# Optimization experiments

Hardware: AMD Instinct MI355X
Metric: run time of the kernel (lower is better)

## Reference

```python
import jax, jax.numpy as jnp
import numpy as np

B = 32; NPG = 290; N = B * NPG; EPG = 2320; E = B * EPG
LP = 900; IN_FEATS = 75; D = 128; HD = 256; K = 3; HK = HD * K; HOUT = 2


def setup_inputs() -> dict:
    key = jax.random.key(0)
    ks = jax.random.split(key, 20)
    s = 0.05
    rng = np.random.default_rng(0)
    off = np.arange(B)[:, None] * NPG  # keep edges inside each graph block
    edge_src = jnp.asarray((rng.integers(0, NPG, (B, EPG)) + off).reshape(-1), dtype=jnp.int32)
    edge_dst = jnp.asarray((rng.integers(0, NPG, (B, EPG)) + off).reshape(-1), dtype=jnp.int32)
    node_h = jax.random.normal(ks[0], (N, IN_FEATS), jnp.float32)
    v_p = jax.random.randint(ks[1], (B, LP), 0, 26, jnp.int32)
    W_init = (jax.random.normal(ks[2], (IN_FEATS, D)) * s).at[:, -1].set(0.0)  # padding unit zeroed
    gcn_W = jax.random.normal(ks[3], (3, 3, D, D)) * s
    gcn_b = jnp.zeros((3, 3, D))
    gcn_Wres = jax.random.normal(ks[4], (3, 3, D, D)) * s
    gcn_bres = jnp.zeros((3, 3, D))
    emb = (jax.random.normal(ks[5], (26, D)) * s).at[0].set(0.0)  # padding_idx=0
    conv1_w = jax.random.normal(ks[6], (D, D, 3)) * s
    conv2_w = jax.random.normal(ks[7], (D, D, 6)) * s
    conv3_w = jax.random.normal(ks[8], (D, D, 9)) * s
    conv_b = jnp.zeros((3, D))
    cnn_bn_g = jnp.ones((3, D)); cnn_bn_b = jnp.zeros((3, D))
    Wv = jax.random.normal(ks[9], (D, HK)) * s; bv = jnp.zeros((HK,))
    Wq = jax.random.normal(ks[10], (D, HK)) * s; bq = jnp.zeros((HK,))
    h_mat = jax.random.normal(ks[11], (HOUT, HK)) * s
    h_bias = jnp.zeros((HOUT,))
    ban_bn_g = jnp.ones((HD,)); ban_bn_b = jnp.zeros((HD,))
    m_w1 = jax.random.normal(ks[12], (HD, 512)) * s; m_b1 = jnp.zeros((512,))
    m_w2 = jax.random.normal(ks[13], (512, 512)) * s; m_b2 = jnp.zeros((512,))
    m_w3 = jax.random.normal(ks[14], (512, 128)) * s; m_b3 = jnp.zeros((128,))
    m_w4 = jax.random.normal(ks[15], (128, 1)) * s; m_b4 = jnp.zeros((1,))
    mbn_g1 = jnp.ones((512,)); mbn_b1 = jnp.zeros((512,))
    mbn_g2 = jnp.ones((512,)); mbn_b2 = jnp.zeros((512,))
    mbn_g3 = jnp.ones((128,)); mbn_b3 = jnp.zeros((128,))
    return dict(node_h=node_h, edge_src=edge_src, edge_dst=edge_dst, v_p=v_p,
                W_init=W_init, gcn_W=gcn_W, gcn_b=gcn_b, gcn_Wres=gcn_Wres, gcn_bres=gcn_bres,
                emb=emb, conv1_w=conv1_w, conv2_w=conv2_w, conv3_w=conv3_w, conv_b=conv_b,
                cnn_bn_g=cnn_bn_g, cnn_bn_b=cnn_bn_b, Wv=Wv, bv=bv, Wq=Wq, bq=bq,
                h_mat=h_mat, h_bias=h_bias, ban_bn_g=ban_bn_g, ban_bn_b=ban_bn_b,
                m_w1=m_w1, m_b1=m_b1, m_w2=m_w2, m_b2=m_b2, m_w3=m_w3, m_b3=m_b3,
                m_w4=m_w4, m_b4=m_b4, mbn_g1=mbn_g1, mbn_b1=mbn_b1, mbn_g2=mbn_g2,
                mbn_b2=mbn_b2, mbn_g3=mbn_g3, mbn_b3=mbn_b3)


def _bn_feat(x, g, b):  # BatchNorm1d on [B, C], training-mode batch stats
    m = jnp.mean(x, 0); v = jnp.var(x, 0)
    return (x - m) * jax.lax.rsqrt(v + 1e-5) * g + b


def _bn_chan(x, g, b):  # BatchNorm1d on [B, C, L]
    m = jnp.mean(x, (0, 2), keepdims=True); v = jnp.var(x, (0, 2), keepdims=True)
    return (x - m) * jax.lax.rsqrt(v + 1e-5) * g[None, :, None] + b[None, :, None]


def _forward(node_h, W_init, gcn_W, gcn_b, gcn_Wres, gcn_bres, emb, conv1_w, conv2_w,
             conv3_w, conv_b, cnn_bn_g, cnn_bn_b, Wv, bv, Wq, bq, h_mat, h_bias,
             ban_bn_g, ban_bn_b, m_w1, m_b1, m_w2, m_b2, m_w3, m_b3, m_w4, m_b4,
             mbn_g1, mbn_b1, mbn_g2, mbn_b2, mbn_g3, mbn_b3, edge_src, edge_dst, v_p):
    relu = jax.nn.relu

    def gcn(h, W, b, Wr, br):  # 3 dgllife GCN layers: sum-aggregate + relu + residual
        for l in range(3):
            agg = jax.ops.segment_sum(h[edge_src], edge_dst, num_segments=N)
            h = relu(agg @ W[l] + b[l]) + relu(h @ Wr[l] + br[l])
        return h

    h0 = node_h @ W_init  # shared init_transform (no bias)
    v_d_o = gcn(h0, gcn_W[0], gcn_b[0], gcn_Wres[0], gcn_bres[0]).reshape(B, NPG, D)
    pos1 = gcn(h0, gcn_W[1], gcn_b[1], gcn_Wres[1], gcn_bres[1]).reshape(B, NPG, D)
    pos2 = gcn(h0, gcn_W[2], gcn_b[2], gcn_Wres[2], gcn_bres[2]).reshape(B, NPG, D)

    x = emb[v_p].transpose(0, 2, 1)  # [B, D, LP]
    dn = ('NCH', 'OIH', 'NCH')
    for w, cb, g, bb in ((conv1_w, conv_b[0], cnn_bn_g[0], cnn_bn_b[0]),
                         (conv2_w, conv_b[1], cnn_bn_g[1], cnn_bn_b[1]),
                         (conv3_w, conv_b[2], cnn_bn_g[2], cnn_bn_b[2])):
        x = jax.lax.conv_general_dilated(x, w, (1,), 'VALID', dimension_numbers=dn) + cb[None, :, None]
        x = _bn_chan(relu(x), g, bb)
    v_p_o = x.transpose(0, 2, 1)  # [B, 885, D]

    q_ = relu(v_p_o @ Wq + bq)  # BAN q_net (shared across views)

    def ban(vd):  # BANLayer forward (eval-mode dropout)
        v_ = relu(vd @ Wv + bv)  # [B, Nv, HK]
        att = jnp.einsum('hk,bvk,bqk->bhvq', h_mat, v_, q_) + h_bias[None, :, None, None]
        f = jnp.einsum('bvk,bhvq,bqk->bk', v_, att, q_)  # summed over h_out heads
        f = f.reshape(-1, HD, K).sum(-1)  # AvgPool1d(k) * k == sum over k groups
        return _bn_feat(f, ban_bn_g, ban_bn_b)

    def mlp(f):
        f = _bn_feat(relu(f @ m_w1 + m_b1), mbn_g1, mbn_b1)
        f = _bn_feat(relu(f @ m_w2 + m_b2), mbn_g2, mbn_b2)
        f = _bn_feat(relu(f @ m_w3 + m_b3), mbn_g3, mbn_b3)
        return f @ m_w4 + m_b4

    f_o = ban(v_d_o)  # Transformer_lar treated as identity -> beta blend is a no-op
    score_o = mlp(f_o)
    s1 = mlp(ban(pos1))
    s2 = mlp(ban(pos2))

    def norm(z):
        return z / jnp.maximum(jnp.linalg.norm(z, axis=1, keepdims=True), 1e-12)

    km = norm(s1) @ norm(s2).T  # cosine_similarity_kernel
    loss = -jnp.mean(jnp.diagonal(jax.nn.log_softmax(km, axis=1)))  # CE vs arange labels
    return jnp.concatenate([score_o, s1, s2, loss * jnp.ones((B, 1), score_o.dtype)], axis=1)


def reference(node_h, edge_src, edge_dst, v_p, W_init, gcn_W, gcn_b, gcn_Wres, gcn_bres,
              emb, conv1_w, conv2_w, conv3_w, conv_b, cnn_bn_g, cnn_bn_b, Wv, bv, Wq, bq,
              h_mat, h_bias, ban_bn_g, ban_bn_b, m_w1, m_b1, m_w2, m_b2, m_w3, m_b3,
              m_w4, m_b4, mbn_g1, mbn_b1, mbn_g2, mbn_b2, mbn_g3, mbn_b3):
    return _forward(node_h, W_init, gcn_W, gcn_b, gcn_Wres, gcn_bres, emb, conv1_w,
                    conv2_w, conv3_w, conv_b, cnn_bn_g, cnn_bn_b, Wv, bv, Wq, bq,
                    h_mat, h_bias, ban_bn_g, ban_bn_b, m_w1, m_b1, m_w2, m_b2, m_w3,
                    m_b3, m_w4, m_b4, mbn_g1, mbn_b1, mbn_g2, mbn_b2, mbn_g3, mbn_b3,
                    edge_src, edge_dst, v_p)
```

## Files before the change

### kernel.cpp

```cpp
#include <hip/hip_runtime.h>
#include <hip/hip_bf16.h>

#define Bc 32
#define NPGc 290
#define Nn 9280
#define Ec 74240
#define LPc 900
#define INFc 75
#define Dd 128
#define HKc 768
#define LQ 885
#define LQP 896
#define S1 904
#define S2 896
#define S3 888
#define NT 78
#define TSZ 4096

typedef __attribute__((ext_vector_type(8))) short bf16x8;
typedef __attribute__((ext_vector_type(16))) float f32x16;

static __device__ __forceinline__ unsigned short f2bf(float v){
  unsigned int u = __float_as_uint(v);
  unsigned int r = u + 0x7FFFu + ((u >> 16) & 1u);
  return (unsigned short)(r >> 16);
}
static __device__ __forceinline__ float bf2f(unsigned short b){
  return __uint_as_float(((unsigned int)b) << 16);
}

__global__ void k_sentinel(float* out, float val){
  int t = threadIdx.x;
  if (t < 128) out[t] = val;
}

__global__ void k_h0(float* __restrict__ h0, const float* __restrict__ nh, const float* __restrict__ Wi){
  int n = blockIdx.x, j = threadIdx.x;
  __shared__ float arow[INFc];
  if (j < INFc) arow[j] = nh[(size_t)n*INFc + j];
  __syncthreads();
  float s = 0.f;
  #pragma unroll 5
  for (int k=0;k<INFc;k++) s += arow[k]*Wi[(size_t)k*Dd + j];
  h0[(size_t)n*Dd + j] = s;
}

__global__ void k_build_adj(float* __restrict__ A, const int* __restrict__ src, const int* __restrict__ dst){
  int e = blockIdx.x*blockDim.x + threadIdx.x;
  if (e >= Ec) return;
  int s = src[e], d = dst[e];
  int b = d / NPGc;
  int dl = d - b*NPGc, sl = s - b*NPGc;
  atomicAdd(&A[((size_t)b*NPGc + dl)*NPGc + sl], 1.f);
}

__global__ void k_wsplit(unsigned short* __restrict__ dstW, unsigned short* __restrict__ dstWr,
                         const float* __restrict__ W, const float* __restrict__ Wr){
  int idx = blockIdx.x*256 + threadIdx.x;
  if (idx >= 9*Dd*Dd) return;
  int gl = idx >> 14;
  int r  = idx & 16383;
  int k  = r >> 7, j = r & 127;
  int c = k >> 4, slot = k & 15;
  size_t o = ((((size_t)gl*8 + c)*Dd + j) << 4) + slot;
  const size_t NW = (size_t)9*8*Dd*16;
  float v = W[idx];
  unsigned short hi = f2bf(v);
  dstW[o] = hi; dstW[NW + o] = f2bf(v - bf2f(hi));
  float u = Wr[idx];
  unsigned short hr = f2bf(u);
  dstWr[o] = hr; dstWr[NW + o] = f2bf(u - bf2f(hr));
}

__global__ void k_aggm(unsigned short* __restrict__ aggH, unsigned short* __restrict__ aggL,
                       const float* __restrict__ inb, size_t istride,
                       const float* __restrict__ Adj){
  int g = blockIdx.z, b = blockIdx.y;
  int i0 = blockIdx.x*64;
  const float* h = inb + (size_t)g*istride + (size_t)b*NPGc*Dd;
  const float* Ab = Adj + (size_t)b*NPGc*NPGc;
  __shared__ unsigned short Bh[128*24], Bl[128*24];
  int tid = threadIdx.x;
  int w = tid>>6, l = tid&63, lr = l&31, lg = l>>5;
  int mh = w>>1, nh = w&1;
  int kr = tid>>4, jq = tid&15;
  f32x16 acc0={}, acc1={};
  for (int c=0;c<19;c++){
    int k0 = c*16;
    {
      int ci = k0 + kr;
      if (ci < NPGc){
        const float* hr_ = h + (size_t)ci*Dd + jq*8;
        #pragma unroll
        for (int m=0;m<8;m++){
          float v = hr_[m];
          unsigned short hi16 = f2bf(v);
          Bh[(jq*8+m)*24 + kr] = hi16;
          Bl[(jq*8+m)*24 + kr] = f2bf(v - bf2f(hi16));
        }
      } else {
        #pragma unroll
        for (int m=0;m<8;m++){ Bh[(jq*8+m)*24+kr]=0; Bl[(jq*8+m)*24+kr]=0; }
      }
    }
    __syncthreads();
    int row = i0 + mh*32 + lr;
    bf16x8 aA = {0,0,0,0,0,0,0,0};
    if (row < NPGc && k0+15 < NPGc){
      const float* ar_ = Ab + (size_t)row*NPGc + k0 + lg*8;
      #pragma unroll
      for (int m=0;m<8;m++) aA[m] = (short)f2bf(ar_[m]);
    } else if (row < NPGc){
      #pragma unroll
      for (int m=0;m<8;m++){
        int k = k0 + lg*8 + m;
        aA[m] = (short)((k < NPGc) ? f2bf(Ab[(size_t)row*NPGc + k]) : 0);
      }
    }
    bf16x8 b0H = *(const bf16x8*)&Bh[(nh*64+lr)*24 + lg*8];
    bf16x8 b0L = *(const bf16x8*)&Bl[(nh*64+lr)*24 + lg*8];
    bf16x8 b1H = *(const bf16x8*)&Bh[(nh*64+32+lr)*24 + lg*8];
    bf16x8 b1L = *(const bf16x8*)&Bl[(nh*64+32+lr)*24 + lg*8];
    acc0 = __builtin_amdgcn_mfma_f32_32x32x16_bf16(aA, b0H, acc0, 0, 0, 0);
    acc0 = __builtin_amdgcn_mfma_f32_32x32x16_bf16(aA, b0L, acc0, 0, 0, 0);
    acc1 = __builtin_amdgcn_mfma_f32_32x32x16_bf16(aA, b1H, acc1, 0, 0, 0);
    acc1 = __builtin_amdgcn_mfma_f32_32x32x16_bf16(aA, b1L, acc1, 0, 0, 0);
    __syncthreads();
  }
  size_t gb = ((size_t)g*Bc + b)*NPGc;
  int j0 = nh*64 + lr;
  #pragma unroll
  for (int reg=0; reg<16; reg++){
    int rowl = (reg&3) + 8*(reg>>2) + 4*lg;
    int i = i0 + mh*32 + rowl;
    if (i < NPGc){
      size_t base = (gb + i)*Dd;
      float v0 = acc0[reg];
      unsigned short h0_ = f2bf(v0);
      aggH[base + j0] = h0_;
      aggL[base + j0] = f2bf(v0 - bf2f(h0_));
      float v1 = acc1[reg];
      unsigned short h1_ = f2bf(v1);
      aggH[base + j0 + 32] = h1_;
      aggL[base + j0 + 32] = f2bf(v1 - bf2f(h1_));
    }
  }
}

__global__ void k_gcnlin(float* __restrict__ outb, size_t ostride,
                         const unsigned short* __restrict__ aggH, const unsigned short* __restrict__ aggL,
                         const float* __restrict__ inb, size_t istride,
                         const unsigned short* __restrict__ WTs, const unsigned short* __restrict__ WrTs,
                         const float* __restrict__ ball, const float* __restrict__ brall, int lno){
  int g = blockIdx.y;
  int m0 = blockIdx.x*64;
  int gl = g*3 + lno;
  const size_t NW = (size_t)9*8*Dd*16;
  int tid = threadIdx.x;
  int w=tid>>6, l=tid&63, lr=l&31, lg=l>>5;
  int mh=w>>1, nh=w&1;
  const float* hin = inb + (size_t)g*istride;
  const unsigned short* agH = aggH + (size_t)g*Nn*Dd;
  const unsigned short* agL = aggL + (size_t)g*Nn*Dd;
  f32x16 aw0={},aw1={},ar0={},ar1={};
  int row = m0 + mh*32 + lr;
  for (int c=0;c<8;c++){
    int k0 = c*16;
    bf16x8 gH = *(const bf16x8*)&agH[(size_t)row*Dd + k0 + lg*8];
    bf16x8 gL = *(const bf16x8*)&agL[(size_t)row*Dd + k0 + lg*8];
    bf16x8 hH, hL;
    {
      const float* hp = hin + (size_t)row*Dd + k0 + lg*8;
      #pragma unroll
      for (int m=0;m<8;m++){
        float v = hp[m];
        unsigned short x = f2bf(v);
        hH[m] = (short)x;
        hL[m] = (short)f2bf(v - bf2f(x));
      }
    }
    size_t wb0 = ((((size_t)gl*8 + c)*Dd) + nh*64 + lr)*16 + (size_t)lg*8;
    size_t wb1 = wb0 + 32*16;
    bf16x8 w0H = *(const bf16x8*)&WTs[wb0];
    bf16x8 w0L = *(const bf16x8*)&WTs[NW + wb0];
    bf16x8 w1H = *(const bf16x8*)&WTs[wb1];
    bf16x8 w1L = *(const bf16x8*)&WTs[NW + wb1];
    bf16x8 r0H = *(const bf16x8*)&WrTs[wb0];
    bf16x8 r0L = *(const bf16x8*)&WrTs[NW + wb0];
    bf16x8 r1H = *(const bf16x8*)&WrTs[wb1];
    bf16x8 r1L = *(const bf16x8*)&WrTs[NW + wb1];
    aw0 = __builtin_amdgcn_mfma_f32_32x32x16_bf16(gH, w0H, aw0, 0,0,0);
    aw0 = __builtin_amdgcn_mfma_f32_32x32x16_bf16(gH, w0L, aw0, 0,0,0);
    aw0 = __builtin_amdgcn_mfma_f32_32x32x16_bf16(gL, w0H, aw0, 0,0,0);
    aw1 = __builtin_amdgcn_mfma_f32_32x32x16_bf16(gH, w1H, aw1, 0,0,0);
    aw1 = __builtin_amdgcn_mfma_f32_32x32x16_bf16(gH, w1L, aw1, 0,0,0);
    aw1 = __builtin_amdgcn_mfma_f32_32x32x16_bf16(gL, w1H, aw1, 0,0,0);
    ar0 = __builtin_amdgcn_mfma_f32_32x32x16_bf16(hH, r0H, ar0, 0,0,0);
    ar0 = __builtin_amdgcn_mfma_f32_32x32x16_bf16(hH, r0L, ar0, 0,0,0);
    ar0 = __builtin_amdgcn_mfma_f32_32x32x16_bf16(hL, r0H, ar0, 0,0,0);
    ar1 = __builtin_amdgcn_mfma_f32_32x32x16_bf16(hH, r1H, ar1, 0,0,0);
    ar1 = __builtin_amdgcn_mfma_f32_32x32x16_bf16(hH, r1L, ar1, 0,0,0);
    ar1 = __builtin_amdgcn_mfma_f32_32x32x16_bf16(hL, r1H, ar1, 0,0,0);
  }
  float* out = outb + (size_t)g*ostride;
  int j0 = nh*64 + lr;
  float b0 = ball[gl*Dd + j0], b1 = ball[gl*Dd + j0 + 32];
  float c0 = brall[gl*Dd + j0], c1 = brall[gl*Dd + j0 + 32];
  #pragma unroll
  for (int reg=0; reg<16; reg++){
    int rowl = (reg&3)+8*(reg>>2)+4*lg;
    int i = m0 + mh*32 + rowl;
    out[(size_t)i*Dd + j0]      = fmaxf(aw0[reg]+b0,0.f) + fmaxf(ar0[reg]+c0,0.f);
    out[(size_t)i*Dd + j0 + 32] = fmaxf(aw1[reg]+b1,0.f) + fmaxf(ar1[reg]+c1,0.f);
  }
}

__global__ void k_embed(float* __restrict__ x, const int* __restrict__ vp, const float* __restrict__ emb){
  int t = blockIdx.x*blockDim.x + threadIdx.x;
  int d = blockIdx.y, b = blockIdx.z;
  if (t >= LPc) return;
  int tok = vp[b*LPc + t];
  x[((size_t)b*Dd + d)*LPc + t] = emb[(size_t)tok*Dd + d];
}

__global__ void k_wpack16(unsigned short* __restrict__ wp, const float* __restrict__ w,
                          const float* __restrict__ scale, int KW, int C){
  int idx = blockIdx.x*256 + threadIdx.x;
  int tot = C*2048;
  if (idx >= tot) return;
  int c = idx >> 11;
  int r = idx & 2047;
  int o = r >> 4, s = r & 15;
  int k = c*16 + s;
  int i = k / KW, kw = k - i*KW;
  float v = w[((size_t)o*Dd + i)*KW + kw];
  if (scale) v *= scale[i];
  unsigned short hi = f2bf(v);
  wp[idx] = hi;
  wp[(size_t)tot + idx] = f2bf(v - bf2f(hi));
}

__global__ void k_bfold(float* __restrict__ bout, const float* __restrict__ w,
                        const float* __restrict__ shf, const float* __restrict__ cb,
                        int go, int KW){
  int o = blockIdx.x, i = threadIdx.x;
  float p = 0.f;
  if (shf){
    const float* wr = w + ((size_t)o*Dd + i)*KW;
    float s = 0.f;
    for (int kw=0; kw<KW; kw++) s += wr[kw];
    p = s * shf[i];
  }
  __shared__ float red[128];
  red[i] = p; __syncthreads();
  for (int st=64; st>0; st>>=1){
    if (i<st) red[i] += red[i+st];
    __syncthreads();
  }
  if (i==0) bout[o] = cb[go+o] + red[0];
}

template<int KW>
__global__ void k_convmfma2(float* __restrict__ y, const float* __restrict__ x,
                            const unsigned short* __restrict__ wp,
                            const float* __restrict__ biasF,
                            int Lout, int XS, int YS){
  const int C = (Dd*KW)/16;
  int b = blockIdx.y;
  int t0 = blockIdx.x*64;
  __shared__ unsigned short Bh[2][64*24], Bl[2][64*24];
  int tid = threadIdx.x;
  int w = tid>>6, l = tid&63, lr = l&31, lg = l>>5;
  int kx = tid&15, tq = tid>>4;
  const unsigned short* wpL = wp + (size_t)C*2048;
  const float* xb = x + (size_t)b*Dd*XS;
  f32x16 acc0={}, acc1={};
  {
    int i = kx/KW, kw = kx - i*KW;
    const float* xr = xb + (size_t)i*XS + t0 + kw + tq*4;
    #pragma unroll
    for (int j=0;j<4;j++){
      float v = xr[j];
      unsigned short h = f2bf(v);
      Bh[0][(tq*4+j)*24+kx] = h;
      Bl[0][(tq*4+j)*24+kx] = f2bf(v - bf2f(h));
    }
  }
  __syncthreads();
  for (int c=0;c<C;c++){
    int cur = c&1, nxt = cur^1;
    bf16x8 aH = *(const bf16x8*)(wp  + ((size_t)c*128 + w*32+lr)*16 + lg*8);
    bf16x8 aL = *(const bf16x8*)(wpL + ((size_t)c*128 + w*32+lr)*16 + lg*8);
    float pv0=0.f,pv1=0.f,pv2=0.f,pv3=0.f;
    if (c+1<C){
      int k1 = (c+1)*16 + kx;
      int i = k1/KW, kw = k1 - i*KW;
      const float* xr = xb + (size_t)i*XS + t0 + kw + tq*4;
      pv0 = xr[0]; pv1 = xr[1]; pv2 = xr[2]; pv3 = xr[3];
    }
    bf16x8 b0H = *(const bf16x8*)&Bh[cur][lr*24 + lg*8];
    bf16x8 b0L = *(const bf16x8*)&Bl[cur][lr*24 + lg*8];
    bf16x8 b1H = *(const bf16x8*)&Bh[cur][(32+lr)*24 + lg*8];
    bf16x8 b1L = *(const bf16x8*)&Bl[cur][(32+lr)*24 + lg*8];
    acc0 = __builtin_amdgcn_mfma_f32_32x32x16_bf16(aH, b0H, acc0, 0,0,0);
    acc1 = __builtin_amdgcn_mfma_f32_32x32x16_bf16(aH, b1H, acc1, 0,0,0);
    acc0 = __builtin_amdgcn_mfma_f32_32x32x16_bf16(aH, b0L, acc0, 0,0,0);
    acc1 = __builtin_amdgcn_mfma_f32_32x32x16_bf16(aH, b1L, acc1, 0,0,0);
    acc0 = __builtin_amdgcn_mfma_f32_32x32x16_bf16(aL, b0H, acc0, 0,0,0);
    acc1 = __builtin_amdgcn_mfma_f32_32x32x16_bf16(aL, b1H, acc1, 0,0,0);
    if (c+1<C){
      unsigned short h;
      h = f2bf(pv0); Bh[nxt][(tq*4+0)*24+kx]=h; Bl[nxt][(tq*4+0)*24+kx]=f2bf(pv0-bf2f(h));
      h = f2bf(pv1); Bh[nxt][(tq*4+1)*24+kx]=h; Bl[nxt][(tq*4+1)*24+kx]=f2bf(pv1-bf2f(h));
      h = f2bf(pv2); Bh[nxt][(tq*4+2)*24+kx]=h; Bl[nxt][(tq*4+2)*24+kx]=f2bf(pv2-bf2f(h));
      h = f2bf(pv3); Bh[nxt][(tq*4+3)*24+kx]=h; Bl[nxt][(tq*4+3)*24+kx]=f2bf(pv3-bf2f(h));
    }
    __syncthreads();
  }
  int tc = t0 + lr;
  #pragma unroll
  for (int reg=0; reg<16; reg++){
    int row = (reg&3) + 8*(reg>>2) + 4*lg;
    int o = w*32 + row;
    float bias = biasF[o];
    float* yp = y + ((size_t)b*Dd + o)*YS;
    if (tc < Lout)      yp[tc]      = fmaxf(acc0[reg] + bias, 0.f);
    if (tc + 32 < Lout) yp[tc + 32] = fmaxf(acc1[reg] + bias, 0.f);
  }
}

__global__ void k_bnc_stats2(float* __restrict__ scale, float* __restrict__ shift,
                             const float* __restrict__ y, int Lout, int YS,
                             const float* __restrict__ g, const float* __restrict__ bb, int go){
  int c = blockIdx.x;
  float s=0.f, ss=0.f;
  int cnt = Bc*Lout;
  for (int i = threadIdx.x; i < cnt; i += blockDim.x){
    int b = i / Lout, t = i - b*Lout;
    float v = y[((size_t)b*Dd+c)*YS + t];
    s += v; ss += v*v;
  }
  __shared__ float rs[256], rss[256];
  rs[threadIdx.x]=s; rss[threadIdx.x]=ss; __syncthreads();
  for (int st=128; st>0; st>>=1){
    if (threadIdx.x<st){ rs[threadIdx.x]+=rs[threadIdx.x+st]; rss[threadIdx.x]+=rss[threadIdx.x+st]; }
    __syncthreads();
  }
  if (threadIdx.x==0){
    float m = rs[0]/cnt; float v = rss[0]/cnt - m*m; if (v<0.f) v=0.f;
    float r = rsqrtf(v+1e-5f);
    float scl = r*g[go+c];
    scale[c] = scl;
    shift[c] = bb[go+c] - m*scl;
  }
}

__global__ void k_qgemm_tile(unsigned short* __restrict__ qTH, unsigned short* __restrict__ qTL,
                             const float* __restrict__ x,
                             const float* __restrict__ W, const float* __restrict__ bias,
                             const float* __restrict__ scale, const float* __restrict__ shift,
                             int gbase){
  int bl = blockIdx.z, b = gbase + bl;
  int m0 = blockIdx.y*64;
  int n0 = blockIdx.x*64;
  __shared__ float As[16][64], Bs[16][64];
  int tid = threadIdx.x;
  int tx = tid & 15, ty = tid >> 4;
  int ldr = tid >> 4, ldc = (tid & 15)*4;
  float acc[4][4] = {};
  for (int k0 = 0; k0 < Dd; k0 += 16){
    int d = k0 + ldr;
    float sc_ = scale[d], sh_ = shift[d];
    const float* xrow = x + ((size_t)b*Dd + d)*S3 + m0 + ldc;
    int mb = m0 + ldc;
    float4 a4;
    a4.x = (mb+0 < LQ) ? xrow[0]*sc_+sh_ : 0.f;
    a4.y = (mb+1 < LQ) ? xrow[1]*sc_+sh_ : 0.f;
    a4.z = (mb+2 < LQ) ? xrow[2]*sc_+sh_ : 0.f;
    a4.w = (mb+3 < LQ) ? xrow[3]*sc_+sh_ : 0.f;
    *(float4*)&As[ldr][ldc] = a4;
    *(float4*)&Bs[ldr][ldc] = *(const float4*)(W + (size_t)d*HKc + n0 + ldc);
    __syncthreads();
    #pragma unroll
    for (int kk=0; kk<16; kk++){
      float a[4], bb[4];
      *(float4*)a  = *(const float4*)&As[kk][ty*4];
      *(float4*)bb = *(const float4*)&Bs[kk][tx*4];
      #pragma unroll
      for (int i=0;i<4;i++)
        #pragma unroll
        for (int j=0;j<4;j++) acc[i][j] += a[i]*bb[j];
    }
    __syncthreads();
  }
  #pragma unroll
  for (int j2=0;j2<4;j2++){
    int n = n0 + tx*4 + j2;
    float bn = bias[n];
    ushort4 sh, sl;
    unsigned short hv[4], lv[4];
    #pragma unroll
    for (int i2=0;i2<4;i2++){
      int m = m0 + ty*4 + i2;
      float v = (m < LQ) ? fmaxf(acc[i2][j2] + bn, 0.f) : 0.f;
      unsigned short h = f2bf(v);
      hv[i2] = h; lv[i2] = f2bf(v - bf2f(h));
    }
    sh.x=hv[0]; sh.y=hv[1]; sh.z=hv[2]; sh.w=hv[3];
    sl.x=lv[0]; sl.y=lv[1]; sl.z=lv[2]; sl.w=lv[3];
    size_t base = ((size_t)bl*HKc + n)*LQP + m0 + ty*4;
    *(ushort4*)(qTH + base) = sh;
    *(ushort4*)(qTL + base) = sl;
  }
}

__global__ void k_colsum_qT(float* __restrict__ S, const unsigned short* __restrict__ qTH,
                            const unsigned short* __restrict__ qTL, int gbase){
  int j = blockIdx.x*256 + threadIdx.x;
  int bl = blockIdx.y;
  if (j >= HKc) return;
  const ushort4* ph = (const ushort4*)(qTH + ((size_t)bl*HKc + j)*LQP);
  const ushort4* pl = (const ushort4*)(qTL + ((size_t)bl*HKc + j)*LQP);
  float s=0.f;
  for (int t=0;t<LQP/4;t++){
    ushort4 a = ph[t], c = pl[t];
    s += bf2f(a.x)+bf2f(a.y)+bf2f(a.z)+bf2f(a.w);
    s += bf2f(c.x)+bf2f(c.y)+bf2f(c.z)+bf2f(c.w);
  }
  S[(gbase+bl)*HKc + j] = s;
}

__global__ void k_gramT(float* __restrict__ Gp, const unsigned short* __restrict__ qTH,
                        const unsigned short* __restrict__ qTL, int gbase){
  int blk = blockIdx.x;
  int bl = blk & 7;
  int tl0 = blk >> 3;
  int bg = gbase + bl;
  int tl = tl0; int ti = 0;
  while (tl >= 12-ti){ tl -= 12-ti; ti++; }
  int tj = ti + tl;
  int r0 = ti*64, c0 = tj*64;
  const unsigned short* qH = qTH + (size_t)bl*HKc*LQP;
  const unsigned short* qL = qTL + (size_t)bl*HKc*LQP;
  float* Gb = Gp + ((size_t)bg*NT + tl0)*TSZ;
  int tid = threadIdx.x;
  int w = tid>>6, l = tid&63, lr = l&31, lg = l>>5;
  int mi = w>>1, ni = w&1;
  const unsigned short* aHp = qH + (size_t)(r0 + mi*32 + lr)*LQP + lg*8;
  const unsigned short* aLp = qL + (size_t)(r0 + mi*32 + lr)*LQP + lg*8;
  const unsigned short* bHp = qH + (size_t)(c0 + ni*32 + lr)*LQP + lg*8;
  const unsigned short* bLp = qL + (size_t)(c0 + ni*32 + lr)*LQP + lg*8;
  f32x16 acc = {};
  #pragma unroll 4
  for (int c=0;c<LQP/16;c++){
    bf16x8 aH = *(const bf16x8*)(aHp + c*16);
    bf16x8 aL = *(const bf16x8*)(aLp + c*16);
    bf16x8 bH = *(const bf16x8*)(bHp + c*16);
    bf16x8 bL = *(const bf16x8*)(bLp + c*16);
    acc = __builtin_amdgcn_mfma_f32_32x32x16_bf16(aH, bH, acc, 0,0,0);
    acc = __builtin_amdgcn_mfma_f32_32x32x16_bf16(aH, bL, acc, 0,0,0);
    acc = __builtin_amdgcn_mfma_f32_32x32x16_bf16(aL, bH, acc, 0,0,0);
  }
  #pragma unroll
  for (int reg=0; reg<16; reg++){
    int row = (reg&3) + 8*(reg>>2) + 4*lg;
    Gb[(size_t)(mi*32+row)*64 + ni*32 + lr] = acc[reg];
  }
}

__global__ void k_vgemm8(float* __restrict__ v, const float* __restrict__ vd,
                         const float* __restrict__ W, const float* __restrict__ bias){
  int j = blockIdx.x*256 + threadIdx.x;
  int r0 = blockIdx.y*8;
  __shared__ float xr[8][Dd];
  for (int idx=threadIdx.x; idx<8*Dd; idx+=256){
    int r = idx>>7, k = idx&127;
    xr[r][k] = vd[(size_t)(r0 + r)*Dd + k];
  }
  __syncthreads();
  float acc[8];
  float bj = bias[j];
  #pragma unroll
  for (int r=0;r<8;r++) acc[r]=bj;
  for (int k=0;k<Dd;k++){
    float wk = W[(size_t)k*HKc+j];
    #pragma unroll
    for (int r=0;r<8;r++) acc[r] += xr[r][k]*wk;
  }
  #pragma unroll
  for (int r=0;r<8;r++)
    v[(size_t)(r0+r)*HKc + j] = fmaxf(acc[r],0.f);
}

__global__ void k_colsum_v(float* __restrict__ S, const float* __restrict__ X){
  int j = blockIdx.x*blockDim.x + threadIdx.x;
  int bl = blockIdx.y;
  if (j >= HKc) return;
  const float* p = X + (size_t)bl*NPGc*HKc + j;
  float s=0.f;
  for (int t=0;t<NPGc;t++) s += p[(size_t)t*HKc];
  S[bl*HKc + j] = s;
}

__global__ void k_gramf_sym(float* __restrict__ f, const float* __restrict__ V,
                            const float* __restrict__ Gp, const float* __restrict__ hm){
  int bg = blockIdx.z;
  int tl0 = blockIdx.x;
  int tl = tl0; int ti = 0;
  while (tl >= 12-ti){ tl -= 12-ti; ti++; }
  int tj = ti + tl;
  int r0 = ti*64, c0 = tj*64;
  int offdiag = (ti != tj);
  const float* Vb = V + (size_t)bg*NPGc*HKc;
  __shared__ float As[16][64], Bs[16][64];
  __shared__ float wc[64], wr[64];
  int tid = threadIdx.x;
  int tx = tid & 15, ty = tid >> 4;
  int ldr = tid >> 4, ldc = (tid & 15)*4;
  if (tid < 64) wc[tid] = hm[c0+tid] + hm[HKc + c0 + tid];
  else if (tid < 128) wr[tid-64] = hm[r0+tid-64] + hm[HKc + r0 + tid-64];
  float acc[4][4] = {};
  for (int t0=0; t0<NPGc; t0+=16){
    float4 av = make_float4(0.f,0.f,0.f,0.f), bv4 = make_float4(0.f,0.f,0.f,0.f);
    if (t0+ldr < NPGc){
      const float* row = Vb + (size_t)(t0+ldr)*HKc;
      av  = *(const float4*)(row + r0 + ldc);
      bv4 = *(const float4*)(row + c0 + ldc);
    }
    *(float4*)&As[ldr][ldc] = av;
    *(float4*)&Bs[ldr][ldc] = bv4;
    __syncthreads();
    #pragma unroll
    for (int tt=0; tt<16; tt++){
      float a[4], bb[4];
      *(float4*)a  = *(const float4*)&As[tt][ty*4];
      *(float4*)bb = *(const float4*)&Bs[tt][tx*4];
      #pragma unroll
      for (int i=0;i<4;i++)
        #pragma unroll
        for (int j=0;j<4;j++) acc[i][j] += a[i]*bb[j];
    }
    __syncthreads();
  }
  const float* gqb = Gp + ((size_t)bg*NT + tl0)*TSZ;
  float w0 = wc[tx*4+0], w1 = wc[tx*4+1], w2 = wc[tx*4+2], w3 = wc[tx*4+3];
  float colp[4] = {0.f,0.f,0.f,0.f};
  #pragma unroll
  for (int i=0;i<4;i++){
    int rl = ty*4 + i;
    int r = r0 + rl;
    const float4 g4 = *(const float4*)(gqb + rl*64 + tx*4);
    float s = acc[i][0]*w0*g4.x + acc[i][1]*w1*g4.y
            + acc[i][2]*w2*g4.z + acc[i][3]*w3*g4.w;
    s += __shfl_xor(s, 1); s += __shfl_xor(s, 2);
    s += __shfl_xor(s, 4); s += __shfl_xor(s, 8);
    if (tx==0) atomicAdd(&f[bg*HKc + r], s);
    if (offdiag){
      float wri = wr[rl];
      colp[0] += acc[i][0]*wri*g4.x;
      colp[1] += acc[i][1]*wri*g4.y;
      colp[2] += acc[i][2]*wri*g4.z;
      colp[3] += acc[i][3]*wri*g4.w;
    }
  }
  if (offdiag){
    #pragma unroll
    for (int j=0;j<4;j++){
      colp[j] += __shfl_xor(colp[j], 16);
      colp[j] += __shfl_xor(colp[j], 32);
    }
    if ((tid & 48) == 0){
      #pragma unroll
      for (int j=0;j<4;j++)
        atomicAdd(&f[bg*HKc + c0 + tx*4 + j], colp[j]);
    }
  }
}

__global__ void k_pool3(float* __restrict__ fp, const float* __restrict__ f3,
                        const float* __restrict__ Sv3, const float* __restrict__ Sq,
                        const float* __restrict__ hb){
  int idx = blockIdx.x*256 + threadIdx.x;
  if (idx >= 3*Bc*256) return;
  int v = idx >> 13;
  int rem = idx & 8191;
  int b = rem >> 8, c = rem & 255;
  const float* f = f3 + (size_t)v*Bc*HKc;
  const float* Sv = Sv3 + (size_t)v*Bc*HKc;
  float hbs = hb[0] + hb[1];
  float s = 0.f;
  #pragma unroll
  for (int r=0;r<3;r++){
    int k = c*3 + r;
    s += f[b*HKc + k] + hbs*Sv[b*HKc + k]*Sq[b*HKc + k];
  }
  fp[idx] = s;
}

__global__ void k_bnfeat3(float* __restrict__ y, const float* __restrict__ x, const float* __restrict__ g,
                          const float* __restrict__ bb, int C){
  int c = blockIdx.x; int v = blockIdx.y; int b = threadIdx.x;
  __shared__ float buf[32];
  __shared__ float mv[2];
  int row = v*32 + b;
  float val = x[(size_t)row*C + c];
  buf[b] = val;
  __syncthreads();
  if (b == 0){
    float s = 0.f;
    for (int i=0;i<32;i++) s += buf[i];
    float m = s/32.f;
    float vs = 0.f;
    for (int i=0;i<32;i++){ float d = buf[i]-m; vs += d*d; }
    mv[0] = m; mv[1] = vs/32.f;
  }
  __syncthreads();
  y[(size_t)row*C + c] = (val - mv[0])*rsqrtf(mv[1]+1e-5f)*g[c] + bb[c];
}

__global__ void k_mlp(float* __restrict__ out, const float* __restrict__ in, const float* __restrict__ W,
                      const float* __restrict__ bias, int K, int Nc, int doRelu){
  int b = blockIdx.y;
  int j = blockIdx.x*blockDim.x + threadIdx.x;
  __shared__ float xr[512];
  for (int k=threadIdx.x; k<K; k+=blockDim.x) xr[k] = in[(size_t)b*K+k];
  __syncthreads();
  if (j >= Nc) return;
  float s = bias[j];
  for (int k=0;k<K;k++) s += xr[k]*W[(size_t)k*Nc + j];
  if (doRelu) s = fmaxf(s, 0.f);
  out[(size_t)b*Nc + j] = s;
}

__global__ void k_score96(float* __restrict__ sc, const float* __restrict__ h, const float* __restrict__ w,
                          const float* __restrict__ bb){
  int b = threadIdx.x; if (b>=96) return;
  float s = bb[0];
  for (int k=0;k<Dd;k++) s += h[(size_t)b*Dd+k]*w[k];
  sc[b] = s;
}

__global__ void k_out(float* __restrict__ out, const float* __restrict__ scores){
  int t = threadIdx.x;
  __shared__ float loss_s;
  if (t == 0){
    float sn1[32], sn2[32];
    for (int i=0;i<32;i++){
      float a = scores[32+i]; sn1[i] = a / fmaxf(fabsf(a), 1e-12f);
      float c = scores[64+i]; sn2[i] = c / fmaxf(fabsf(c), 1e-12f);
    }
    float acc = 0.f;
    for (int i=0;i<32;i++){
      float mx = -1e30f;
      for (int j=0;j<32;j++) mx = fmaxf(mx, sn1[i]*sn2[j]);
      float se = 0.f;
      for (int j=0;j<32;j++) se += expf(sn1[i]*sn2[j]-mx);
      acc += sn1[i]*sn2[i] - (mx + logf(se));
    }
    loss_s = -acc/32.f;
  }
  __syncthreads();
  out[t*4+0] = scores[t];
  out[t*4+1] = scores[32+t];
  out[t*4+2] = scores[64+t];
  out[t*4+3] = loss_s;
}

extern "C" void kernel_launch(void* const* d_in, const int* in_sizes, int n_in,
                              void* d_out, int out_size, void* d_ws, size_t ws_size,
                              hipStream_t stream){
  static const int exp_sizes[38] = {
    Nn*INFc, Ec, Ec, Bc*LPc, INFc*Dd,
    9*Dd*Dd, 9*Dd, 9*Dd*Dd, 9*Dd,
    26*Dd, Dd*Dd*3, Dd*Dd*6, Dd*Dd*9, 3*Dd, 3*Dd, 3*Dd,
    Dd*HKc, HKc, Dd*HKc, HKc, 2*HKc, 2, 256, 256,
    256*512, 512, 512*512, 512, 512*128, 128, 128, 1,
    512, 512, 512, 512, 128, 128 };
  if (n_in != 38){ k_sentinel<<<1,128,0,stream>>>((float*)d_out, 2000.f + n_in); return; }
  for (int i=0;i<38;i++){
    if (in_sizes[i] != exp_sizes[i]){
      k_sentinel<<<1,128,0,stream>>>((float*)d_out, 1000.f + i); return;
    }
  }

  const float* node_h=(const float*)d_in[0];
  const int*  esrc  =(const int*)d_in[1];
  const int*  edst  =(const int*)d_in[2];
  const int*  vp    =(const int*)d_in[3];
  const float* W_init=(const float*)d_in[4];
  const float* gcn_W =(const float*)d_in[5];
  const float* gcn_b =(const float*)d_in[6];
  const float* gcn_Wr=(const float*)d_in[7];
  const float* gcn_br=(const float*)d_in[8];
  const float* emb   =(const float*)d_in[9];
  const float* c1w=(const float*)d_in[10];
  const float* c2w=(const float*)d_in[11];
  const float* c3w=(const float*)d_in[12];
  const float* cbv=(const float*)d_in[13];
  const float* bng=(const float*)d_in[14];
  const float* bnb=(const float*)d_in[15];
  const float* Wv =(const float*)d_in[16];
  const float* bvv=(const float*)d_in[17];
  const float* Wq =(const float*)d_in[18];
  const float* bq =(const float*)d_in[19];
  const float* hmat =(const float*)d_in[20];
  const float* hbias=(const float*)d_in[21];
  const float* bang =(const float*)d_in[22];
  const float* banb =(const float*)d_in[23];
  const float* mw1=(const float*)d_in[24]; const float* mb1=(const float*)d_in[25];
  const float* mw2=(const float*)d_in[26]; const float* mb2=(const float*)d_in[27];
  const float* mw3=(const float*)d_in[28]; const float* mb3=(const float*)d_in[29];
  const float* mw4=(const float*)d_in[30]; const float* mb4=(const float*)d_in[31];
  const float* g1=(const float*)d_in[32]; const float* bb1=(const float*)d_in[33];
  const float* g2=(const float*)d_in[34]; const float* bb2=(const float*)d_in[35];
  const float* g3=(const float*)d_in[36]; const float* bb3=(const float*)d_in[37];

  float* ws = (float*)d_ws;
  size_t off = 0;
  auto alloc = [&](size_t n){ float* p = ws + off; off += n; return p; };

  const size_t NDsz = (size_t)Nn*Dd;
  const size_t CNNBP = (size_t)Bc*Dd*S1;
  const size_t ADJ  = (size_t)Bc*NPGc*NPGc;
  const size_t QTF  = (size_t)8*HKc*LQP;
  const size_t VB   = (size_t)Bc*NPGc*HKc;
  const size_t AGGF = (size_t)3*Nn*Dd;
  size_t ARENA = 7*NDsz + ADJ + AGGF;
  if (ARENA < 4*NDsz + VB) ARENA = 4*NDsz + VB;
  if (ARENA < CNNBP + QTF) ARENA = CNNBP + QTF;
  if (ARENA < 2*CNNBP) ARENA = 2*CNNBP;

  float* Sq   = alloc((size_t)Bc*HKc);
  float* Sv3  = alloc((size_t)3*Bc*HKc);
  float* fbuf3= alloc((size_t)3*Bc*HKc);
  float* fpool3=alloc((size_t)3*Bc*256);
  float* hh1  = alloc((size_t)96*512);
  float* hh2  = alloc((size_t)96*512);
  float* hh3  = alloc((size_t)96*128);
  float* sc   = alloc(96);
  float* scl1 = alloc(128); float* shf1 = alloc(128);
  float* scl2 = alloc(128); float* shf2 = alloc(128);
  float* scl3 = alloc(128); float* shf3 = alloc(128);
  float* b1f  = alloc(128); float* b2f  = alloc(128); float* b3f = alloc(128);
  unsigned short* wp1 = (unsigned short*)alloc((size_t)384*128);
  unsigned short* wp2 = (unsigned short*)alloc((size_t)768*128);
  unsigned short* wp3 = (unsigned short*)alloc((size_t)1152*128);
  unsigned short* WTs  = (unsigned short*)alloc(147456);
  unsigned short* WrTs = (unsigned short*)alloc(147456);
  float* Gqp = alloc((size_t)Bc*NT*TSZ);
  float* arena = alloc(ARENA);

  float* cnnA = arena;
  float* cnnB = arena + CNNBP;
  float* qbuf = arena + CNNBP;
  unsigned short* qTH = (unsigned short*)qbuf;
  unsigned short* qTL = qTH + (size_t)8*HKc*LQP;
  float* h0b  = arena;
  float* Bb   = arena + NDsz;
  float* Cb   = arena + 4*NDsz;
  float* Adj  = arena + 7*NDsz;
  unsigned short* aggH = (unsigned short*)(arena + 7*NDsz + ADJ);
  unsigned short* aggL = aggH + (size_t)3*Nn*Dd;
  float* vbuf = arena + 4*NDsz;

  k_wpack16<<<(24*2048+255)/256,256,0,stream>>>(wp1, c1w, nullptr, 3, 24);
  k_bfold<<<128,128,0,stream>>>(b1f, c1w, nullptr, cbv, 0, 3);
  k_wsplit<<<(9*Dd*Dd+255)/256,256,0,stream>>>(WTs, WrTs, gcn_W, gcn_Wr);

  k_embed<<<dim3((LPc+127)/128, Dd, Bc),128,0,stream>>>(cnnB, vp, emb);
  k_convmfma2<3><<<dim3(15,Bc),256,0,stream>>>(cnnA, cnnB, wp1, b1f, 898, 900, S1);
  k_bnc_stats2<<<Dd,256,0,stream>>>(scl1, shf1, cnnA, 898, S1, bng, bnb, 0);
  k_wpack16<<<(48*2048+255)/256,256,0,stream>>>(wp2, c2w, scl1, 6, 48);
  k_bfold<<<128,128,0,stream>>>(b2f, c2w, shf1, cbv, 128, 6);
  k_convmfma2<6><<<dim3(14,Bc),256,0,stream>>>(cnnB, cnnA, wp2, b2f, 893, S1, S2);
  k_bnc_stats2<<<Dd,256,0,stream>>>(scl2, shf2, cnnB, 893, S2, bng, bnb, 128);
  k_wpack16<<<(72*2048+255)/256,256,0,stream>>>(wp3, c3w, scl2, 9, 72);
  k_bfold<<<128,128,0,stream>>>(b3f, c3w, shf2, cbv, 256, 9);
  k_convmfma2<9><<<dim3(14,Bc),256,0,stream>>>(cnnA, cnnB, wp3, b3f, 885, S2, S3);
  k_bnc_stats2<<<Dd,256,0,stream>>>(scl3, shf3, cnnA, 885, S3, bng, bnb, 256);

  for (int gb = 0; gb < Bc; gb += 8){
    k_qgemm_tile<<<dim3(12,LQP/64,8),256,0,stream>>>(qTH, qTL, cnnA, Wq, bq, scl3, shf3, gb);
    k_colsum_qT<<<dim3(3,8),256,0,stream>>>(Sq, qTH, qTL, gb);
    k_gramT<<<NT*8,256,0,stream>>>(Gqp, qTH, qTL, gb);
  }

  hipMemsetAsync(Adj, 0, ADJ*sizeof(float), stream);
  k_build_adj<<<(Ec+255)/256,256,0,stream>>>(Adj, esrc, edst);

  hipMemsetAsync(fbuf3, 0, (size_t)3*Bc*HKc*sizeof(float), stream);

  k_h0<<<Nn,Dd,0,stream>>>(h0b, node_h, W_init);
  k_aggm<<<dim3(5,Bc,3),256,0,stream>>>(aggH, aggL, h0b, 0, Adj);
  k_gcnlin<<<dim3(145,3),256,0,stream>>>(Bb, NDsz, aggH, aggL, h0b, 0, WTs, WrTs, gcn_b, gcn_br, 0);
  k_aggm<<<dim3(5,Bc,3),256,0,stream>>>(aggH, aggL, Bb, NDsz, Adj);
  k_gcnlin<<<dim3(145,3),256,0,stream>>>(Cb, NDsz, aggH, aggL, Bb, NDsz, WTs, WrTs, gcn_b, gcn_br, 1);
  k_aggm<<<dim3(5,Bc,3),256,0,stream>>>(aggH, aggL, Cb, NDsz, Adj);
  k_gcnlin<<<dim3(145,3),256,0,stream>>>(Bb, NDsz, aggH, aggL, Cb, NDsz, WTs, WrTs, gcn_b, gcn_br, 2);

  for (int g=0; g<3; g++){
    k_vgemm8<<<dim3(3,(Bc*NPGc)/8),256,0,stream>>>(vbuf, Bb + (size_t)g*NDsz, Wv, bvv);
    k_colsum_v<<<dim3(3,Bc),256,0,stream>>>(Sv3 + (size_t)g*Bc*HKc, vbuf);
    k_gramf_sym<<<dim3(NT,1,Bc),256,0,stream>>>(fbuf3 + (size_t)g*Bc*HKc, vbuf, Gqp, hmat);
  }

  k_pool3<<<(3*Bc*256+255)/256,256,0,stream>>>(fpool3, fbuf3, Sv3, Sq, hbias);
  k_bnfeat3<<<dim3(256,3),32,0,stream>>>(fpool3, fpool3, bang, banb, 256);
  k_mlp<<<dim3(2,96),256,0,stream>>>(hh1, fpool3, mw1, mb1, 256, 512, 1);
  k_bnfeat3<<<dim3(512,3),32,0,stream>>>(hh1, hh1, g1, bb1, 512);
  k_mlp<<<dim3(2,96),256,0,stream>>>(hh2, hh1, mw2, mb2, 512, 512, 1);
  k_bnfeat3<<<dim3(512,3),32,0,stream>>>(hh2, hh2, g2, bb2, 512);
  k_mlp<<<dim3(1,96),256,0,stream>>>(hh3, hh2, mw3, mb3, 512, 128, 1);
  k_bnfeat3<<<dim3(128,3),32,0,stream>>>(hh3, hh3, g3, bb3, 128);
  k_score96<<<1,96,0,stream>>>(sc, hh3, mw4, mb4);
  k_out<<<1,32,0,stream>>>((float*)d_out, sc);
}
```

Baseline: 1.763 ms.

## Move drug-side V GEMM and Gram product to split-bf16 MFMA with transposed layout

Replaces the scalar FP32 V projection and the FP32 shared-memory Gram kernel with MFMA-based kernels that use a three-product hi/lo bf16 split to keep near-FP32 accuracy. The V projection now writes V transposed and padded to 320 rows as hi/lo bf16, so the Gram kernel can load contiguous bf16x8 fragments straight from global memory. Column sums are taken from the split representation. This trades extra MFMA passes and a scattered transposed store for removing the FP32 FMA-bound inner loops.

New measurement: 1.884 ms. 6.8% more time.

```diff
diff --git a/kernel.cpp b/kernel.cpp
--- a/kernel.cpp
+++ b/kernel.cpp
@@ -11,6 +11,7 @@
 #define HKc 768
 #define LQ 885
 #define LQP 896
+#define NPP 320
 #define S1 904
 #define S2 896
 #define S3 888
@@ -70,6 +71,18 @@
   float u = Wr[idx];
   unsigned short hr = f2bf(u);
   dstWr[o] = hr; dstWr[NW + o] = f2bf(u - bf2f(hr));
+}
+
+__global__ void k_wsplitV(unsigned short* __restrict__ dst, const float* __restrict__ W){
+  int idx = blockIdx.x*256 + threadIdx.x;
+  if (idx >= Dd*HKc) return;
+  int k = idx / HKc, j = idx - k*HKc;
+  int c = k >> 4, slot = k & 15;
+  size_t o = (((size_t)c*HKc + j) << 4) + slot;
+  const size_t NWv = (size_t)8*HKc*16;
+  float v = W[idx];
+  unsigned short hi = f2bf(v);
+  dst[o] = hi; dst[NWv + o] = f2bf(v - bf2f(hi));
 }
 
 __global__ void k_aggm(unsigned short* __restrict__ aggH, unsigned short* __restrict__ aggL,
@@ -468,42 +481,79 @@
   }
 }
 
-__global__ void k_vgemm8(float* __restrict__ v, const float* __restrict__ vd,
-                         const float* __restrict__ W, const float* __restrict__ bias){
+__global__ void k_vgemmT(unsigned short* __restrict__ vTH, unsigned short* __restrict__ vTL,
+                         const float* __restrict__ vd, const unsigned short* __restrict__ WvTs,
+                         const float* __restrict__ bias){
+  int g = blockIdx.z;
+  int m0 = blockIdx.x*64;
+  int n0 = blockIdx.y*64;
+  const float* hin = vd + (size_t)g*NPGc*Dd;
+  const size_t NWv = (size_t)8*HKc*16;
+  int tid = threadIdx.x;
+  int w=tid>>6, l=tid&63, lr=l&31, lg=l>>5;
+  int mi=w>>1, ni=w&1;
+  f32x16 acc={};
+  int row = m0 + mi*32 + lr;
+  bool rok = row < NPGc;
+  for (int c=0;c<8;c++){
+    bf16x8 hH={0,0,0,0,0,0,0,0}, hL={0,0,0,0,0,0,0,0};
+    if (rok){
+      const float* hp = hin + (size_t)row*Dd + c*16 + lg*8;
+      #pragma unroll
+      for (int m=0;m<8;m++){
+        float v = hp[m];
+        unsigned short x = f2bf(v);
+        hH[m] = (short)x;
+        hL[m] = (short)f2bf(v - bf2f(x));
+      }
+    }
+    size_t wb = (((size_t)c*HKc + n0 + ni*32 + lr) << 4) + lg*8;
+    bf16x8 wH = *(const bf16x8*)&WvTs[wb];
+    bf16x8 wL = *(const bf16x8*)&WvTs[NWv + wb];
+    acc = __builtin_amdgcn_mfma_f32_32x32x16_bf16(hH, wH, acc, 0,0,0);
+    acc = __builtin_amdgcn_mfma_f32_32x32x16_bf16(hH, wL, acc, 0,0,0);
+    acc = __builtin_amdgcn_mfma_f32_32x32x16_bf16(hL, wH, acc, 0,0,0);
+  }
+  __shared__ float tile[4][32][33];
+  float bn = bias[n0 + ni*32 + lr];
+  #pragma unroll
+  for (int reg=0; reg<16; reg++){
+    int pat = (reg&3) + 8*(reg>>2) + 4*lg;
+    tile[w][pat][lr] = fmaxf(acc[reg] + bn, 0.f);
+  }
+  __syncthreads();
+  unsigned short* oH = vTH + (size_t)g*HKc*NPP;
+  unsigned short* oL = vTL + (size_t)g*HKc*NPP;
+  int mg = m0 + mi*32 + lr;
+  bool mok = mg < NPGc;
+  for (int j=0;j<32;j++){
+    float val = mok ? tile[w][lr][j] : 0.f;
+    int ng = n0 + ni*32 + j;
+    unsigned short h = f2bf(val);
+    oH[(size_t)ng*NPP + mg] = h;
+    oL[(size_t)ng*NPP + mg] = f2bf(val - bf2f(h));
+  }
+}
+
+__global__ void k_colsum_vT(float* __restrict__ S, const unsigned short* __restrict__ vTH,
+                            const unsigned short* __restrict__ vTL){
   int j = blockIdx.x*256 + threadIdx.x;
-  int r0 = blockIdx.y*8;
-  __shared__ float xr[8][Dd];
-  for (int idx=threadIdx.x; idx<8*Dd; idx+=256){
-    int r = idx>>7, k = idx&127;
-    xr[r][k] = vd[(size_t)(r0 + r)*Dd + k];
-  }
-  __syncthreads();
-  float acc[8];
-  float bj = bias[j];
-  #pragma unroll
-  for (int r=0;r<8;r++) acc[r]=bj;
-  for (int k=0;k<Dd;k++){
-    float wk = W[(size_t)k*HKc+j];
-    #pragma unroll
-    for (int r=0;r<8;r++) acc[r] += xr[r][k]*wk;
-  }
-  #pragma unroll
-  for (int r=0;r<8;r++)
-    v[(size_t)(r0+r)*HKc + j] = fmaxf(acc[r],0.f);
-}
-
-__global__ void k_colsum_v(float* __restrict__ S, const float* __restrict__ X){
-  int j = blockIdx.x*blockDim.x + threadIdx.x;
   int bl = blockIdx.y;
   if (j >= HKc) return;
-  const float* p = X + (size_t)bl*NPGc*HKc + j;
+  const ushort4* ph = (const ushort4*)(vTH + ((size_t)bl*HKc + j)*NPP);
+  const ushort4* pl = (const ushort4*)(vTL + ((size_t)bl*HKc + j)*NPP);
   float s=0.f;
-  for (int t=0;t<NPGc;t++) s += p[(size_t)t*HKc];
+  for (int t=0;t<NPP/4;t++){
+    ushort4 a = ph[t], c = pl[t];
+    s += bf2f(a.x)+bf2f(a.y)+bf2f(a.z)+bf2f(a.w);
+    s += bf2f(c.x)+bf2f(c.y)+bf2f(c.z)+bf2f(c.w);
+  }
   S[bl*HKc + j] = s;
 }
 
-__global__ void k_gramf_sym(float* __restrict__ f, const float* __restrict__ V,
-                            const float* __restrict__ Gp, const float* __restrict__ hm){
+__global__ void k_gramfT(float* __restrict__ f, const unsigned short* __restrict__ vTH,
+                         const unsigned short* __restrict__ vTL,
+                         const float* __restrict__ Gp, const float* __restrict__ hm){
   int bg = blockIdx.z;
   int tl0 = blockIdx.x;
   int tl = tl0; int ti = 0;
@@ -511,69 +561,47 @@
   int tj = ti + tl;
   int r0 = ti*64, c0 = tj*64;
   int offdiag = (ti != tj);
-  const float* Vb = V + (size_t)bg*NPGc*HKc;
-  __shared__ float As[16][64], Bs[16][64];
-  __shared__ float wc[64], wr[64];
+  const unsigned short* vH = vTH + (size_t)bg*HKc*NPP;
+  const unsigned short* vL = vTL + (size_t)bg*HKc*NPP;
+  const float* Gb = Gp + ((size_t)bg*NT + tl0)*TSZ;
   int tid = threadIdx.x;
-  int tx = tid & 15, ty = tid >> 4;
-  int ldr = tid >> 4, ldc = (tid & 15)*4;
-  if (tid < 64) wc[tid] = hm[c0+tid] + hm[HKc + c0 + tid];
-  else if (tid < 128) wr[tid-64] = hm[r0+tid-64] + hm[HKc + r0 + tid-64];
-  float acc[4][4] = {};
-  for (int t0=0; t0<NPGc; t0+=16){
-    float4 av = make_float4(0.f,0.f,0.f,0.f), bv4 = make_float4(0.f,0.f,0.f,0.f);
-    if (t0+ldr < NPGc){
-      const float* row = Vb + (size_t)(t0+ldr)*HKc;
-      av  = *(const float4*)(row + r0 + ldc);
-      bv4 = *(const float4*)(row + c0 + ldc);
-    }
-    *(float4*)&As[ldr][ldc] = av;
-    *(float4*)&Bs[ldr][ldc] = bv4;
-    __syncthreads();
-    #pragma unroll
-    for (int tt=0; tt<16; tt++){
-      float a[4], bb[4];
-      *(float4*)a  = *(const float4*)&As[tt][ty*4];
-      *(float4*)bb = *(const float4*)&Bs[tt][tx*4];
-      #pragma unroll
-      for (int i=0;i<4;i++)
-        #pragma unroll
-        for (int j=0;j<4;j++) acc[i][j] += a[i]*bb[j];
-    }
-    __syncthreads();
-  }
-  const float* gqb = Gp + ((size_t)bg*NT + tl0)*TSZ;
-  float w0 = wc[tx*4+0], w1 = wc[tx*4+1], w2 = wc[tx*4+2], w3 = wc[tx*4+3];
-  float colp[4] = {0.f,0.f,0.f,0.f};
+  int w = tid>>6, l = tid&63, lr = l&31, lg = l>>5;
+  int mi = w>>1, ni = w&1;
+  const unsigned short* aHp = vH + (size_t)(r0 + mi*32 + lr)*NPP + lg*8;
+  const unsigned short* aLp = vL + (size_t)(r0 + mi*32 + lr)*NPP + lg*8;
+  const unsigned short* bHp = vH + (size_t)(c0 + ni*32 + lr)*NPP + lg*8;
+  const unsigned short* bLp = vL + (size_t)(c0 + ni*32 + lr)*NPP + lg*8;
+  f32x16 acc = {};
+  #pragma unroll 4
+  for (int c=0;c<NPP/16;c++){
+    bf16x8 aH = *(const bf16x8*)(aHp + c*16);
+    bf16x8 aL = *(const bf16x8*)(aLp + c*16);
+    bf16x8 bH = *(const bf16x8*)(bHp + c*16);
+    bf16x8 bL = *(const bf16x8*)(bLp + c*16);
+    acc = __builtin_amdgcn_mfma_f32_32x32x16_bf16(aH, bH, acc, 0,0,0);
+    acc = __builtin_amdgcn_mfma_f32_32x32x16_bf16(aH, bL, acc, 0,0,0);
+    acc = __builtin_amdgcn_mfma_f32_32x32x16_bf16(aL, bH, acc, 0,0,0);
+  }
+  int colg = c0 + ni*32 + lr;
+  float wcv = hm[colg] + hm[HKc + colg];
+  float colp = 0.f;
   #pragma unroll
-  for (int i=0;i<4;i++){
-    int rl = ty*4 + i;
-    int r = r0 + rl;
-    const float4 g4 = *(const float4*)(gqb + rl*64 + tx*4);
-    float s = acc[i][0]*w0*g4.x + acc[i][1]*w1*g4.y
-            + acc[i][2]*w2*g4.z + acc[i][3]*w3*g4.w;
+  for (int reg=0; reg<16; reg++){
+    int rloc = mi*32 + (reg&3) + 8*(reg>>2) + 4*lg;
+    float gq = Gb[(size_t)rloc*64 + ni*32 + lr];
+    float val = acc[reg]*gq;
+    float s = val * wcv;
     s += __shfl_xor(s, 1); s += __shfl_xor(s, 2);
-    s += __shfl_xor(s, 4); s += __shfl_xor(s, 8);
-    if (tx==0) atomicAdd(&f[bg*HKc + r], s);
+    s += __shfl_xor(s, 4); s += __shfl_xor(s, 8); s += __shfl_xor(s, 16);
+    if (lr == 0) atomicAdd(&f[bg*HKc + r0 + rloc], s);
     if (offdiag){
-      float wri = wr[rl];
-      colp[0] += acc[i][0]*wri*g4.x;
-      colp[1] += acc[i][1]*wri*g4.y;
-      colp[2] += acc[i][2]*wri*g4.z;
-      colp[3] += acc[i][3]*wri*g4.w;
+      float wrv = hm[r0 + rloc] + hm[HKc + r0 + rloc];
+      colp += val * wrv;
     }
   }
   if (offdiag){
-    #pragma unroll
-    for (int j=0;j<4;j++){
-      colp[j] += __shfl_xor(colp[j], 16);
-      colp[j] += __shfl_xor(colp[j], 32);
-    }
-    if ((tid & 48) == 0){
-      #pragma unroll
-      for (int j=0;j<4;j++)
-        atomicAdd(&f[bg*HKc + c0 + tx*4 + j], colp[j]);
-    }
+    colp += __shfl_xor(colp, 32);
+    if (lg == 0) atomicAdd(&f[bg*HKc + colg], colp);
   }
 }
 
@@ -723,10 +751,10 @@
   const size_t CNNBP = (size_t)Bc*Dd*S1;
   const size_t ADJ  = (size_t)Bc*NPGc*NPGc;
   const size_t QTF  = (size_t)8*HKc*LQP;
-  const size_t VB   = (size_t)Bc*NPGc*HKc;
+  const size_t VTF  = (size_t)Bc*HKc*NPP;
   const size_t AGGF = (size_t)3*Nn*Dd;
   size_t ARENA = 7*NDsz + ADJ + AGGF;
-  if (ARENA < 4*NDsz + VB) ARENA = 4*NDsz + VB;
+  if (ARENA < 4*NDsz + VTF) ARENA = 4*NDsz + VTF;
   if (ARENA < CNNBP + QTF) ARENA = CNNBP + QTF;
   if (ARENA < 2*CNNBP) ARENA = 2*CNNBP;
 
@@ -747,6 +775,7 @@
   unsigned short* wp3 = (unsigned short*)alloc((size_t)1152*128);
   unsigned short* WTs  = (unsigned short*)alloc(147456);
   unsigned short* WrTs = (unsigned short*)alloc(147456);
+  unsigned short* WvTs = (unsigned short*)alloc(98304);
   float* Gqp = alloc((size_t)Bc*NT*TSZ);
   float* arena = alloc(ARENA);
 
@@ -761,11 +790,13 @@
   float* Adj  = arena + 7*NDsz;
   unsigned short* aggH = (unsigned short*)(arena + 7*NDsz + ADJ);
   unsigned short* aggL = aggH + (size_t)3*Nn*Dd;
-  float* vbuf = arena + 4*NDsz;
+  unsigned short* vTH = (unsigned short*)(arena + 4*NDsz);
+  unsigned short* vTL = vTH + (size_t)Bc*HKc*NPP;
 
   k_wpack16<<<(24*2048+255)/256,256,0,stream>>>(wp1, c1w, nullptr, 3, 24);
   k_bfold<<<128,128,0,stream>>>(b1f, c1w, nullptr, cbv, 0, 3);
   k_wsplit<<<(9*Dd*Dd+255)/256,256,0,stream>>>(WTs, WrTs, gcn_W, gcn_Wr);
+  k_wsplitV<<<(Dd*HKc+255)/256,256,0,stream>>>(WvTs, Wv);
 
   k_embed<<<dim3((LPc+127)/128, Dd, Bc),128,0,stream>>>(cnnB, vp, emb);
   k_convmfma2<3><<<dim3(15,Bc),256,0,stream>>>(cnnA, cnnB, wp1, b1f, 898, 900, S1);
@@ -799,9 +830,9 @@
   k_gcnlin<<<dim3(145,3),256,0,stream>>>(Bb, NDsz, aggH, aggL, Cb, NDsz, WTs, WrTs, gcn_b, gcn_br, 2);
 
   for (int g=0; g<3; g++){
-    k_vgemm8<<<dim3(3,(Bc*NPGc)/8),256,0,stream>>>(vbuf, Bb + (size_t)g*NDsz, Wv, bvv);
-    k_colsum_v<<<dim3(3,Bc),256,0,stream>>>(Sv3 + (size_t)g*Bc*HKc, vbuf);
-    k_gramf_sym<<<dim3(NT,1,Bc),256,0,stream>>>(fbuf3 + (size_t)g*Bc*HKc, vbuf, Gqp, hmat);
+    k_vgemmT<<<dim3(NPP/64,HKc/64,Bc),256,0,stream>>>(vTH, vTL, Bb + (size_t)g*NDsz, WvTs, bvv);
+    k_colsum_vT<<<dim3(3,Bc),256,0,stream>>>(Sv3 + (size_t)g*Bc*HKc, vTH, vTL);
+    k_gramfT<<<dim3(NT,1,Bc),256,0,stream>>>(fbuf3 + (size_t)g*Bc*HKc, vTH, vTL, Gqp, hmat);
   }
 
   k_pool3<<<(3*Bc*256+255)/256,256,0,stream>>>(fpool3, fbuf3, Sv3, Sq, hbias);
```
